# Kernel tuning notes

Hardware: AMD Instinct MI355X
Metric: run time of the kernel (lower is better)

## Reference

```python
import jax, jax.numpy as jnp
import numpy as np

EPS = 1e-12  # matches torch F.normalize default eps

def setup_inputs() -> dict:
    key = jax.random.key(0)
    k1, k2, k3, k4 = jax.random.split(key, 4)
    B, C, H, W = 4, 256, 32, 32
    D, K = 2048, 16384
    return {
        "hidden_states": jax.random.normal(k1, (B, C, H, W), dtype=jnp.float32),
        "codebook": jax.random.normal(k2, (K, D), dtype=jnp.float32),
        "qc_w": jax.random.normal(k3, (D, C), dtype=jnp.float32) * 0.02,
        "qc_b": jax.random.normal(k4, (D,), dtype=jnp.float32) * 0.02,
    }

def _l2norm(x):
    # F.normalize(p=2, dim=-1): x / max(||x||, eps)
    n = jnp.sqrt(jnp.sum(x * x, axis=-1, keepdims=True))
    return x / jnp.maximum(n, EPS)

def reference(hidden_states, codebook, qc_w, qc_b):
    B, C, H, W = hidden_states.shape
    D = qc_w.shape[0]
    # quant_conv: 1x1 conv == per-pixel linear projection C -> D
    h = jnp.einsum("bchw,dc->bdhw", hidden_states, qc_w) + qc_b[None, :, None, None]
    # flatten to tokens: (B*H*W, D)
    flat = h.transpose(0, 2, 3, 1).reshape(-1, D)
    hn = _l2norm(flat)                  # (N, D)
    en = _l2norm(codebook)              # (K, D)
    sim = hn @ en.T                     # (N, K) cosine similarity
    idx = jnp.argmax(sim, axis=1)       # (N,)
    quant = en[idx]                     # gather normalized codes
    quant = quant.reshape(B, H, W, D).transpose(0, 3, 1, 2)
    return quant, idx
```

## Files before the change

### kernel.cpp

```cpp
#include <hip/hip_runtime.h>
#include <hip/hip_fp16.h>
#include <stdint.h>

#define NTOK 4096
#define KCB  16384
#define CAP  64
#define MARGIN_C 0.02f
#define MARGIN_F 0.02f

typedef _Float16 f16;
typedef _Float16 f16x8 __attribute__((ext_vector_type(8)));
typedef float f32x4 __attribute__((ext_vector_type(4)));

typedef const __attribute__((address_space(1))) uint32_t* gptr_t;
typedef __attribute__((address_space(3))) uint32_t* lptr_t;
__device__ __forceinline__ void gload_lds16(const void* g, void* l) {
  __builtin_amdgcn_global_load_lds((gptr_t)g, (lptr_t)l, 16, 0, 0);
}

__device__ __forceinline__ unsigned encf(float f) {
  unsigned u = __float_as_uint(f);
  return (u & 0x80000000u) ? ~u : (u | 0x80000000u);
}
__device__ __forceinline__ float decf(unsigned e) {
  return (e & 0x80000000u) ? __uint_as_float(e ^ 0x80000000u) : __uint_as_float(~e);
}

__global__ void k_init(unsigned* smax, int* cnt) {
  int i = blockIdx.x * 256 + threadIdx.x;
  if (i < NTOK) { smax[i] = 0u; cnt[i] = 0; }
}

__global__ __launch_bounds__(256) void k_build_wT(const float* qc_w, const float* qc_b, f16* wT) {
  __shared__ float tl[64][65];
  int d0 = blockIdx.x * 64, c0 = blockIdx.y * 64;
  int jj = threadIdx.x & 63, i0 = threadIdx.x >> 6;
  for (int ii = 0; ii < 64; ii += 4) {
    int i = ii + i0; int d = d0 + i; int c = c0 + jj;
    float v = 0.f;
    if (c < 256) v = qc_w[(size_t)d * 256 + c];
    else if (c == 256) v = qc_b[d];
    tl[i][jj] = v;
  }
  __syncthreads();
  for (int jj2 = 0; jj2 < 64; jj2 += 4) {
    int j = jj2 + i0; int i = threadIdx.x & 63;
    wT[(size_t)(c0 + j) * 2048 + d0 + i] = (f16)tl[i][j];
  }
}

__global__ __launch_bounds__(256) void k_build_x(const float* hid, f16* x16, float* x32) {
  __shared__ float tl[64][65];
  int hw0 = blockIdx.x * 64, c0 = blockIdx.y * 64, b = blockIdx.z;
  int jj = threadIdx.x & 63, i0 = threadIdx.x >> 6;
  for (int ii = 0; ii < 64; ii += 4) {
    int i = ii + i0;
    tl[i][jj] = hid[((size_t)b * 256 + c0 + i) * 1024 + hw0 + jj];
  }
  __syncthreads();
  for (int jj2 = 0; jj2 < 64; jj2 += 4) {
    int j = jj2 + i0; int i = threadIdx.x & 63;
    int t = b * 1024 + hw0 + j; float v = tl[i][j];
    x32[(size_t)t * 256 + c0 + i] = v;
    x16[(size_t)t * 320 + c0 + i] = (f16)v;
  }
  if (blockIdx.y == 0) {
    int tb = b * 1024 + hw0;
    for (int q = 0; q < 16; q++) {
      int idx2 = threadIdx.x * 16 + q;
      int tl2 = idx2 >> 6, p = idx2 & 63;
      x16[(size_t)(tb + tl2) * 320 + 256 + p] = (p == 0) ? (f16)1.0f : (f16)0.0f;
    }
  }
}

__global__ __launch_bounds__(256) void k_proj2b(const float* x32, const float* qc_w, const float* qc_b, double* h64) {
  __shared__ double At[16][128];
  __shared__ double Bt[16][16][9];
  int t0 = blockIdx.y * 128, d0 = blockIdx.x * 128;
  int tid = threadIdx.x;
  int tr = tid >> 4, dc = tid & 15;
  int srow = tid & 127, kh = (tid >> 7) * 8;
  int sg = srow >> 3, se = srow & 7;
  const float* pA = x32 + (size_t)(t0 + srow) * 256 + kh;
  const float* pB = qc_w + (size_t)(d0 + srow) * 256 + kh;
  f32x4 a0 = *(const f32x4*)pA, a1 = *(const f32x4*)(pA + 4);
  f32x4 b0 = *(const f32x4*)pB, b1 = *(const f32x4*)(pB + 4);
  double acc[8][8] = {};
  for (int kk = 0; kk < 256; kk += 16) {
    __syncthreads();
#pragma unroll
    for (int j = 0; j < 4; j++) {
      At[kh + j][srow] = (double)a0[j]; At[kh + 4 + j][srow] = (double)a1[j];
      Bt[kh + j][sg][se] = (double)b0[j]; Bt[kh + 4 + j][sg][se] = (double)b1[j];
    }
    __syncthreads();
    if (kk + 16 < 256) {
      a0 = *(const f32x4*)(pA + kk + 16); a1 = *(const f32x4*)(pA + kk + 20);
      b0 = *(const f32x4*)(pB + kk + 16); b1 = *(const f32x4*)(pB + kk + 20);
    }
#pragma unroll
    for (int k = 0; k < 16; k++) {
      double a[8], b[8];
#pragma unroll
      for (int j = 0; j < 8; j++) a[j] = At[k][tr * 8 + j];
#pragma unroll
      for (int j = 0; j < 8; j++) b[j] = Bt[k][dc][j];
#pragma unroll
      for (int i = 0; i < 8; i++)
#pragma unroll
        for (int j = 0; j < 8; j++)
          acc[i][j] = fma(a[i], b[j], acc[i][j]);
    }
  }
#pragma unroll
  for (int i = 0; i < 8; i++)
#pragma unroll
    for (int j = 0; j < 8; j++) {
      int col = d0 + dc * 8 + j;
      h64[(size_t)(t0 + tr * 8 + i) * 2048 + col] = acc[i][j] + (double)qc_b[col];
    }
}

__global__ __launch_bounds__(256) void k_pgemm4(const float* cb, const f16* wT, f16* P16kt,
                                                double* inv64, float* inv32) {
  __shared__ f16 Al[2][64][32];
  __shared__ f16 Bl[2][160][32];
  __shared__ double nsum[64][4];
  __shared__ double invsh[64];
  int j0 = blockIdx.x * 64;
  int c0 = blockIdx.y * 160;
  int tid = threadIdx.x, wid = tid >> 6, lane = tid & 63;
  int cl = lane & 15, g = lane >> 4;
  f32x4 acc[10];
#pragma unroll
  for (int n = 0; n < 10; n++) acc[n] = (f32x4)0.0f;
  int arow = tid & 63, aseg = tid >> 6;
  double s2 = 0.0;

  auto aload = [&](int kk, f32x4& v0, f32x4& v1) {
    v0 = *(const f32x4*)(cb + (size_t)(j0 + arow) * 2048 + kk + aseg * 8);
    v1 = *(const f32x4*)(cb + (size_t)(j0 + arow) * 2048 + kk + aseg * 8 + 4);
  };
  auto addnorm = [&](f32x4 v0, f32x4 v1) {
#pragma unroll
    for (int e = 0; e < 4; e++) {
      s2 += (double)v0[e] * (double)v0[e];
      s2 += (double)v1[e] * (double)v1[e];
    }
  };
  auto awrite = [&](int buf, f32x4 v0, f32x4 v1) {
    f16x8 h;
#pragma unroll
    for (int e = 0; e < 4; e++) { h[e] = (f16)v0[e]; h[4 + e] = (f16)v1[e]; }
    int sp = aseg ^ ((arow >> 1) & 3);
    *(f16x8*)((char*)&Al[buf][arow][0] + sp * 16) = h;
  };
  auto stageB = [&](int kk, int buf) {
#pragma unroll
    for (int i = 0; i < 3; i++) {
      int g2 = wid + 4 * i;
      if (g2 < 10) {
        int r0 = 16 * g2;
        int rl = r0 + (lane >> 2);
        int sl = (lane & 3) ^ ((rl >> 1) & 3);
        gload_lds16(wT + (size_t)(c0 + rl) * 2048 + kk + sl * 8, &Bl[buf][r0][0]);
      }
    }
  };
  auto rdA = [&](int buf, int r, int sg2) -> f16x8 {
    return *(const f16x8*)((const char*)&Al[buf][0][0] + r * 64 + ((sg2 ^ ((r >> 1) & 3)) << 4));
  };
  auto rdB = [&](int buf, int r, int sg2) -> f16x8 {
    return *(const f16x8*)((const char*)&Bl[buf][0][0] + r * 64 + ((sg2 ^ ((r >> 1) & 3)) << 4));
  };

  { f32x4 v0, v1; aload(0, v0, v1); addnorm(v0, v1); awrite(0, v0, v1); }
  stageB(0, 0);
  asm volatile("s_waitcnt vmcnt(0)" ::: "memory");
  __syncthreads();
  for (int s = 0; s < 64; s++) {
    int buf = s & 1;
    f32x4 v0, v1;
    if (s < 63) { aload((s + 1) * 32, v0, v1); stageB((s + 1) * 32, buf ^ 1); }
    f16x8 av = rdA(buf, 16 * wid + cl, g);
#pragma unroll
    for (int n = 0; n < 10; n++) {
      f16x8 bv = rdB(buf, 16 * n + cl, g);
      acc[n] = __builtin_amdgcn_mfma_f32_16x16x32_f16(av, bv, acc[n], 0, 0, 0);
    }
    if (s < 63) { addnorm(v0, v1); awrite(buf ^ 1, v0, v1); }
    asm volatile("s_waitcnt vmcnt(0)" ::: "memory");
    __syncthreads();
  }
  nsum[arow][aseg] = s2;
  __syncthreads();
  if (tid < 64) {
    double t = nsum[tid][0] + nsum[tid][1] + nsum[tid][2] + nsum[tid][3];
    double nn = sqrt(t); nn = fmax(nn, 1e-12);
    double iv = 1.0 / nn;
    invsh[tid] = iv;
    if (blockIdx.y == 0) { inv64[j0 + tid] = iv; inv32[j0 + tid] = (float)iv; }
  }
  __syncthreads();
#pragma unroll
  for (int r = 0; r < 4; r++) {
    int rloc = 16 * wid + 4 * g + r;
    int row = j0 + rloc;
    float sc = (float)invsh[rloc];
#pragma unroll
    for (int n = 0; n < 10; n++) {
      int c = c0 + 16 * n + cl;
      int ks = c >> 5;
      int sl = ((c & 31) >> 3) ^ ((row >> 1) & 3);
      P16kt[(((size_t)ks * KCB + row) << 5) + (sl << 3) + (c & 7)] = (f16)(acc[n][r] * sc);
    }
  }
}

template <int PASS>
__global__ __launch_bounds__(256) void k_screen7(const f16* x16, const f16* P16kt,
                                                 unsigned* smax, int* cnt, float* cand_v, int* cand_i) {
  __shared__ f16 Al[3][128][32];
  __shared__ f16 Bl[3][128][32];
  int bid = blockIdx.x;
  int nb = ((bid & 7) << 4) | ((bid >> 3) & 15);
  int tb = bid >> 7;
  int n0 = nb * 128, t0 = tb * 128;
  int tid = threadIdx.x, wid = tid >> 6, lane = tid & 63;
  int wr = wid >> 1, wc = wid & 1;
  int cl = lane & 15, g = lane >> 4;
  f32x4 acc[4][4];
#pragma unroll
  for (int m = 0; m < 4; m++)
#pragma unroll
    for (int n = 0; n < 4; n++) acc[m][n] = (f32x4)0.0f;

  auto stageA = [&](int ks, int buf) {
#pragma unroll
    for (int i = 0; i < 2; i++) {
      int r0 = 32 * wid + 16 * i;
      int rl = r0 + (lane >> 2);
      int sl = (lane & 3) ^ ((rl >> 1) & 3);
      gload_lds16(x16 + (size_t)(t0 + rl) * 320 + ks * 32 + sl * 8, &Al[buf][r0][0]);
    }
  };
  auto stageB = [&](int ks, int buf) {
    const f16* src = P16kt + (((size_t)ks * KCB + n0) << 5) + wid * 1024 + lane * 8;
    gload_lds16(src, &Bl[buf][wid * 32][0]);
    gload_lds16(src + 512, &Bl[buf][wid * 32 + 16][0]);
  };
  auto rdA = [&](int buf, int r, int sg) -> f16x8 {
    return *(const f16x8*)((const char*)&Al[buf][0][0] + r * 64 + ((sg ^ ((r >> 1) & 3)) << 4));
  };
  auto rdB = [&](int buf, int r, int sg) -> f16x8 {
    return *(const f16x8*)((const char*)&Bl[buf][0][0] + r * 64 + ((sg ^ ((r >> 1) & 3)) << 4));
  };

  stageA(0, 0); stageB(0, 0);
#pragma unroll
  for (int s = 0; s < 10; s++) {
    const int buf = s % 3;
    if (s < 9) {
      const int nb2 = (s + 1) % 3;
      stageA(s + 1, nb2); stageB(s + 1, nb2);
      asm volatile("s_waitcnt vmcnt(4)" ::: "memory");
    } else {
      asm volatile("s_waitcnt vmcnt(0)" ::: "memory");
    }
    __builtin_amdgcn_s_barrier();
    __builtin_amdgcn_sched_barrier(0);
    f16x8 av[4], bv[4];
#pragma unroll
    for (int m = 0; m < 4; m++) av[m] = rdA(buf, 64 * wr + 16 * m + cl, g);
#pragma unroll
    for (int n = 0; n < 4; n++) bv[n] = rdB(buf, 64 * wc + 16 * n + cl, g);
#pragma unroll
    for (int m = 0; m < 4; m++)
#pragma unroll
      for (int n = 0; n < 4; n++)
        acc[m][n] = __builtin_amdgcn_mfma_f32_16x16x32_f16(av[m], bv[n], acc[m][n], 0, 0, 0);
  }

  if (PASS == 0) {
#pragma unroll
    for (int m = 0; m < 4; m++) {
#pragma unroll
      for (int r = 0; r < 4; r++) {
        float v = -3.4e38f;
#pragma unroll
        for (int n = 0; n < 4; n++) v = fmaxf(v, acc[m][n][r]);
        v = fmaxf(v, __shfl_xor(v, 1));
        v = fmaxf(v, __shfl_xor(v, 2));
        v = fmaxf(v, __shfl_xor(v, 4));
        v = fmaxf(v, __shfl_xor(v, 8));
        if (cl == 0) {
          int row = t0 + 64 * wr + 16 * m + 4 * g + r;
          atomicMax(&smax[row], encf(v));
        }
      }
    }
  } else {
#pragma unroll
    for (int m = 0; m < 4; m++) {
#pragma unroll
      for (int r = 0; r < 4; r++) {
        int row = t0 + 64 * wr + 16 * m + 4 * g + r;
        float lim = decf(smax[row]) - MARGIN_C;
#pragma unroll
        for (int n = 0; n < 4; n++) {
          float vv = acc[m][n][r];
          if (vv >= lim) {
            int slot = atomicAdd(&cnt[row], 1);
            if (slot < CAP) { cand_v[row * CAP + slot] = vv; cand_i[row * CAP + slot] = n0 + 64 * wc + 16 * n + cl; }
          }
        }
      }
    }
  }
}

__global__ __launch_bounds__(256) void k_rescore2(const double* h64, const float* cb, const double* inv64,
                                                  const int* cnt, const float* cand_v, const int* cand_i,
                                                  float* idxf, int* idxi) {
  __shared__ double hsh[2048];
  __shared__ double red[256];
  __shared__ int redi[256];
  __shared__ float wmax[4];
  int t = blockIdx.x, tid = threadIdx.x;
  int lane = tid & 63, wid = tid >> 6;
  for (int i = 0; i < 8; i++) hsh[tid + 256 * i] = h64[(size_t)t * 2048 + tid + 256 * i];
  __syncthreads();
  int ctot = cnt[t];
  double bV = -1e300; int bI = 0x7fffffff;
  if (ctot <= CAP) {
    int n = ctot;
    float gm = -3.4e38f;
    for (int c = tid; c < n; c += 256) gm = fmaxf(gm, cand_v[t * CAP + c]);
    for (int o = 32; o; o >>= 1) gm = fmaxf(gm, __shfl_xor(gm, o));
    if (lane == 0) wmax[wid] = gm;
    __syncthreads();
    float gmax = fmaxf(fmaxf(wmax[0], wmax[1]), fmaxf(wmax[2], wmax[3]));
    float lim = gmax - MARGIN_F;
    for (int c = 0; c < n; c++) {
      float v = cand_v[t * CAP + c];
      if (v < lim) continue;
      int code = cand_i[t * CAP + c];
      const float* row = cb + (size_t)code * 2048;
      double p = 0.0;
      for (int i = 0; i < 8; i++) { int d = tid + 256 * i; p += hsh[d] * (double)row[d]; }
      red[tid] = p; __syncthreads();
      for (int s2 = 128; s2; s2 >>= 1) { if (tid < s2) red[tid] += red[tid + s2]; __syncthreads(); }
      if (tid == 0) {
        double sv = red[0] * inv64[code];
        if (sv > bV || (sv == bV && code < bI)) { bV = sv; bI = code; }
      }
      __syncthreads();
    }
  } else {
    for (int code = tid; code < KCB; code += 256) {
      const float* row = cb + (size_t)code * 2048;
      double p = 0.0;
      for (int d = 0; d < 2048; d++) p += hsh[d] * (double)row[d];
      double sv = p * inv64[code];
      if (sv > bV || (sv == bV && code < bI)) { bV = sv; bI = code; }
    }
    red[tid] = bV; redi[tid] = bI; __syncthreads();
    for (int s2 = 128; s2; s2 >>= 1) {
      if (tid < s2) {
        double ov = red[tid + s2]; int oi = redi[tid + s2];
        if (ov > red[tid] || (ov == red[tid] && oi < redi[tid])) { red[tid] = ov; redi[tid] = oi; }
      }
      __syncthreads();
    }
    if (tid == 0) { bV = red[0]; bI = redi[0]; }
  }
  if (tid == 0) { idxi[t] = bI; idxf[t] = (float)bI; }
}

__global__ __launch_bounds__(256) void k_quant(const float* cb, const float* inv32, const int* idxi, float* out0) {
  int hw = blockIdx.x * 256 + threadIdx.x;
  int d = blockIdx.y, b = blockIdx.z;
  int t = b * 1024 + hw;
  int row = idxi[t];
  out0[((size_t)b * 2048 + d) * 1024 + hw] = cb[(size_t)row * 2048 + d] * inv32[row];
}

extern "C" void kernel_launch(void* const* d_in, const int* in_sizes, int n_in,
                              void* d_out, int out_size, void* d_ws, size_t ws_size,
                              hipStream_t stream) {
  const float* hid = (const float*)d_in[0];
  const float* cb  = (const float*)d_in[1];
  const float* qw  = (const float*)d_in[2];
  const float* qb  = (const float*)d_in[3];
  float* out = (float*)d_out;

  char* w = (char*)d_ws;
  size_t off = 0;
  auto alloc = [&](size_t bytes) -> void* {
    void* p = w + off;
    off += (bytes + 255) & ~(size_t)255;
    return p;
  };
  double* h64   = (double*)alloc((size_t)NTOK * 2048 * 8);
  f16*    x16   = (f16*)   alloc((size_t)NTOK * 320 * 2);
  float*  x32   = (float*) alloc((size_t)NTOK * 256 * 4);
  f16*    wT    = (f16*)   alloc((size_t)320 * 2048 * 2);
  f16*    P16kt = (f16*)   alloc((size_t)10 * KCB * 32 * 2);
  double* inv64 = (double*)alloc((size_t)KCB * 8);
  float*  inv32 = (float*) alloc((size_t)KCB * 4);
  unsigned* smax= (unsigned*)alloc((size_t)NTOK * 4);
  int*    cnt   = (int*)   alloc((size_t)NTOK * 4);
  float*  cand_v= (float*) alloc((size_t)NTOK * CAP * 4);
  int*    cand_i= (int*)   alloc((size_t)NTOK * CAP * 4);
  int*    idxi  = (int*)   alloc((size_t)NTOK * 4);

  k_init<<<16, 256, 0, stream>>>(smax, cnt);
  k_build_wT<<<dim3(32, 5), 256, 0, stream>>>(qw, qb, wT);
  k_build_x<<<dim3(16, 4, 4), 256, 0, stream>>>(hid, x16, x32);
  k_proj2b<<<dim3(16, 32), 256, 0, stream>>>(x32, qw, qb, h64);
  k_pgemm4<<<dim3(256, 2), 256, 0, stream>>>(cb, wT, P16kt, inv64, inv32);
  k_screen7<0><<<4096, 256, 0, stream>>>(x16, P16kt, smax, cnt, cand_v, cand_i);
  k_screen7<1><<<4096, 256, 0, stream>>>(x16, P16kt, smax, cnt, cand_v, cand_i);
  k_rescore2<<<NTOK, 256, 0, stream>>>(h64, cb, inv64, cnt, cand_v, cand_i, out + 8388608, idxi);
  k_quant<<<dim3(4, 2048, 4), 256, 0, stream>>>(cb, inv32, idxi, out);
}
```

Measured before the change: 426.6 us.

## Fuse two-pass screening into one pass using block-local row maxima

Replaces the two screening launches (a global atomic row max, then candidate collection) with a single kernel. That kernel computes each row's max within its own 128-column tile in shared memory and collects candidates within a margin of that local max. Candidate capacity rises from 64 to 256 per token, and the global smax buffer and its encode/decode helpers are removed. This saves one full fp16 GEMM pass over the codebook. In exchange, every tile now contributes at least one candidate per row, so the rescoring kernel must process far more candidates. The per-token capacity may also overflow and drop the true argmax.

```diff
diff --git a/kernel.cpp b/kernel.cpp
--- a/kernel.cpp
+++ b/kernel.cpp
@@ -4,7 +4,7 @@
 
 #define NTOK 4096
 #define KCB  16384
-#define CAP  64
+#define CAP  256
 #define MARGIN_C 0.02f
 #define MARGIN_F 0.02f
 
@@ -18,17 +18,9 @@
   __builtin_amdgcn_global_load_lds((gptr_t)g, (lptr_t)l, 16, 0, 0);
 }
 
-__device__ __forceinline__ unsigned encf(float f) {
-  unsigned u = __float_as_uint(f);
-  return (u & 0x80000000u) ? ~u : (u | 0x80000000u);
-}
-__device__ __forceinline__ float decf(unsigned e) {
-  return (e & 0x80000000u) ? __uint_as_float(e ^ 0x80000000u) : __uint_as_float(~e);
-}
-
-__global__ void k_init(unsigned* smax, int* cnt) {
+__global__ void k_init(int* cnt) {
   int i = blockIdx.x * 256 + threadIdx.x;
-  if (i < NTOK) { smax[i] = 0u; cnt[i] = 0; }
+  if (i < NTOK) cnt[i] = 0;
 }
 
 __global__ __launch_bounds__(256) void k_build_wT(const float* qc_w, const float* qc_b, f16* wT) {
@@ -218,11 +210,11 @@
   }
 }
 
-template <int PASS>
-__global__ __launch_bounds__(256) void k_screen7(const f16* x16, const f16* P16kt,
-                                                 unsigned* smax, int* cnt, float* cand_v, int* cand_i) {
+__global__ __launch_bounds__(256) void k_screen8(const f16* x16, const f16* P16kt,
+                                                 int* cnt, float* cand_v, int* cand_i) {
   __shared__ f16 Al[3][128][32];
   __shared__ f16 Bl[3][128][32];
+  __shared__ float smx[128][2];
   int bid = blockIdx.x;
   int nb = ((bid & 7) << 4) | ((bid >> 3) & 15);
   int tb = bid >> 7;
@@ -282,38 +274,34 @@
         acc[m][n] = __builtin_amdgcn_mfma_f32_16x16x32_f16(av[m], bv[n], acc[m][n], 0, 0, 0);
   }
 
-  if (PASS == 0) {
-#pragma unroll
-    for (int m = 0; m < 4; m++) {
-#pragma unroll
-      for (int r = 0; r < 4; r++) {
-        float v = -3.4e38f;
-#pragma unroll
-        for (int n = 0; n < 4; n++) v = fmaxf(v, acc[m][n][r]);
-        v = fmaxf(v, __shfl_xor(v, 1));
-        v = fmaxf(v, __shfl_xor(v, 2));
-        v = fmaxf(v, __shfl_xor(v, 4));
-        v = fmaxf(v, __shfl_xor(v, 8));
-        if (cl == 0) {
-          int row = t0 + 64 * wr + 16 * m + 4 * g + r;
-          atomicMax(&smax[row], encf(v));
-        }
-      }
-    }
-  } else {
-#pragma unroll
-    for (int m = 0; m < 4; m++) {
-#pragma unroll
-      for (int r = 0; r < 4; r++) {
-        int row = t0 + 64 * wr + 16 * m + 4 * g + r;
-        float lim = decf(smax[row]) - MARGIN_C;
-#pragma unroll
-        for (int n = 0; n < 4; n++) {
-          float vv = acc[m][n][r];
-          if (vv >= lim) {
-            int slot = atomicAdd(&cnt[row], 1);
-            if (slot < CAP) { cand_v[row * CAP + slot] = vv; cand_i[row * CAP + slot] = n0 + 64 * wc + 16 * n + cl; }
-          }
+#pragma unroll
+  for (int m = 0; m < 4; m++) {
+#pragma unroll
+    for (int r = 0; r < 4; r++) {
+      float v = -3.4e38f;
+#pragma unroll
+      for (int n = 0; n < 4; n++) v = fmaxf(v, acc[m][n][r]);
+      v = fmaxf(v, __shfl_xor(v, 1));
+      v = fmaxf(v, __shfl_xor(v, 2));
+      v = fmaxf(v, __shfl_xor(v, 4));
+      v = fmaxf(v, __shfl_xor(v, 8));
+      if (cl == 0) smx[64 * wr + 16 * m + 4 * g + r][wc] = v;
+    }
+  }
+  __syncthreads();
+#pragma unroll
+  for (int m = 0; m < 4; m++) {
+#pragma unroll
+    for (int r = 0; r < 4; r++) {
+      int rloc = 64 * wr + 16 * m + 4 * g + r;
+      float lim = fmaxf(smx[rloc][0], smx[rloc][1]) - MARGIN_C;
+      int row = t0 + rloc;
+#pragma unroll
+      for (int n = 0; n < 4; n++) {
+        float vv = acc[m][n][r];
+        if (vv >= lim) {
+          int slot = atomicAdd(&cnt[row], 1);
+          if (slot < CAP) { cand_v[row * CAP + slot] = vv; cand_i[row * CAP + slot] = n0 + 64 * wc + 16 * n + cl; }
         }
       }
     }
@@ -409,19 +397,17 @@
   f16*    P16kt = (f16*)   alloc((size_t)10 * KCB * 32 * 2);
   double* inv64 = (double*)alloc((size_t)KCB * 8);
   float*  inv32 = (float*) alloc((size_t)KCB * 4);
-  unsigned* smax= (unsigned*)alloc((size_t)NTOK * 4);
   int*    cnt   = (int*)   alloc((size_t)NTOK * 4);
   float*  cand_v= (float*) alloc((size_t)NTOK * CAP * 4);
   int*    cand_i= (int*)   alloc((size_t)NTOK * CAP * 4);
   int*    idxi  = (int*)   alloc((size_t)NTOK * 4);
 
-  k_init<<<16, 256, 0, stream>>>(smax, cnt);
+  k_init<<<16, 256, 0, stream>>>(cnt);
   k_build_wT<<<dim3(32, 5), 256, 0, stream>>>(qw, qb, wT);
   k_build_x<<<dim3(16, 4, 4), 256, 0, stream>>>(hid, x16, x32);
   k_proj2b<<<dim3(16, 32), 256, 0, stream>>>(x32, qw, qb, h64);
   k_pgemm4<<<dim3(256, 2), 256, 0, stream>>>(cb, wT, P16kt, inv64, inv32);
-  k_screen7<0><<<4096, 256, 0, stream>>>(x16, P16kt, smax, cnt, cand_v, cand_i);
-  k_screen7<1><<<4096, 256, 0, stream>>>(x16, P16kt, smax, cnt, cand_v, cand_i);
+  k_screen8<<<4096, 256, 0, stream>>>(x16, P16kt, cnt, cand_v, cand_i);
   k_rescore2<<<NTOK, 256, 0, stream>>>(h64, cb, inv64, cnt, cand_v, cand_i, out + 8388608, idxi);
   k_quant<<<dim3(4, 2048, 4), 256, 0, stream>>>(cb, inv32, idxi, out);
 }
```

Result: slower. 572.9 us (+34.3%).
